# Kernel tuning notes

Measured on AMD Instinct MI355X. Metric: run time of the kernel, lower is better.

## Reference

```python
import jax, jax.numpy as jnp
import numpy as np

B, LAT, H, K = 8, 128, 1024, 294
N, E = 100000, 1600000
XSIZE = 128.0
TAU = 0.5
STEPS = 3


def setup_inputs() -> dict:
    key = jax.random.key(0)
    ks = jax.random.split(key, 20)
    s_in = 1.0 / np.sqrt(LAT)
    s_h = 1.0 / np.sqrt(H)
    inp = {
        "latent": jax.random.normal(ks[0], (B, LAT), jnp.float32),
        "W0": jax.random.normal(ks[1], (LAT, H), jnp.float32) * s_in,
        "b0": jnp.zeros((H,), jnp.float32),
        "W1": jax.random.normal(ks[2], (H, H), jnp.float32) * s_h,
        "b1": jnp.zeros((H,), jnp.float32),
        "W2": jax.random.normal(ks[3], (H, H), jnp.float32) * s_h,
        "b2": jnp.zeros((H,), jnp.float32),
        "W3": jax.random.normal(ks[4], (H, H), jnp.float32) * s_h,
        "b3": jnp.zeros((H,), jnp.float32),
        # coefficient heads use normal(1e-4) init in the source
        "Wx": jax.random.normal(ks[5], (H, K), jnp.float32) * 1e-4,
        "bx": jnp.zeros((K,), jnp.float32),
        "Wy": jax.random.normal(ks[6], (H, K), jnp.float32) * 1e-4,
        "by": jnp.zeros((K,), jnp.float32),
        "Wz": jax.random.normal(ks[7], (H, K), jnp.float32) * 1e-4,
        "bz": jnp.zeros((K,), jnp.float32),
        # precomputed Zernike/spherical basis evaluated at the N coords: [K, N]
        "Z": jax.random.normal(ks[8], (K, N), jnp.float32),
        "edge_weights": jax.random.uniform(ks[9], (E,), jnp.float32),
        "edge_index": jax.random.randint(ks[10], (2, E), 0, N, jnp.int64),
    }
    return inp


def _decode_coefficients(latent, W0, b0, W1, b1, W2, b2, W3, b3,
                         Wx, bx, Wy, by, Wz, bz):
    h = jax.nn.relu(latent @ W0 + b0)
    for W, b in ((W1, b1), (W2, b2), (W3, b3)):
        h = jax.nn.relu(h + h @ W + b)  # residual MLP block
    return h @ Wx + bx, h @ Wy + by, h @ Wz + bz  # [B, K] each


def _diffuse(flow, edge_index, edge_weights):
    """Graph diffusion smoothing of per-node vectors. flow: [B, N, 3]."""
    src, dst = edge_index[0], edge_index[1]
    deg = jax.ops.segment_sum(edge_weights, dst, num_segments=N)
    deg = jnp.maximum(deg, 1e-6)[:, None, None]  # [N,1,1]
    f = jnp.transpose(flow, (1, 0, 2))  # [N, B, 3]
    w = edge_weights[:, None, None]
    for _ in range(STEPS):
        msg = f[src] * w                                        # gather  [E,B,3]
        agg = jax.ops.segment_sum(msg, dst, num_segments=N)     # scatter [N,B,3]
        f = (1.0 - TAU) * f + TAU * agg / deg
    return jnp.transpose(f, (1, 0, 2))  # [B, N, 3]


def reference(latent, W0, b0, W1, b1, W2, b2, W3, b3,
              Wx, bx, Wy, by, Wz, bz, Z, edge_weights, edge_index):
    cx, cy, cz = _decode_coefficients(latent, W0, b0, W1, b1, W2, b2, W3, b3,
                                      Wx, bx, Wy, by, Wz, bz)
    # basis evaluation: per-axis coefficients contracted with Zernike basis
    dx = jnp.einsum("bk,kn->bn", cx, Z)
    dy = jnp.einsum("bk,kn->bn", cy, Z)
    dz = jnp.einsum("bk,kn->bn", cz, Z)
    flow = (0.5 * XSIZE) * jnp.stack([dx, dy, dz], axis=-1)  # [B, N, 3]
    flow = _diffuse(flow, edge_index, edge_weights)
    reg = 1e-4 * jnp.sqrt(jnp.sum(cx ** 2 + cy ** 2 + cz ** 2))
    return flow, reg
```

## Files before the change

### kernel.cpp

```cpp
#include <hip/hip_runtime.h>
#include <math.h>

#define BB 8
#define LAT 128
#define HH 1024
#define KK 294
#define NN 100000
#define EE 1600000
#define NSTEPS 3
#define XS_HALF 64.0f

#define NB 391
#define CS 8
#define COB 28
#define COB2 30
#define EPT 8
#define EST 200000
#define EBLK 782
#define GON 40

#define F3NB 391
#define KPAD 320

__constant__ float ccoefT[KPAD * 24];


__device__ __forceinline__ void mlp_part_body(int bid, const float* __restrict__ hin,
                                              const float* __restrict__ W,
                                              float* __restrict__ part, int jdim) {
    int it = bid & 15;
    int bs = bid >> 4;
    int tx = threadIdx.x;
    int il = tx & 63;
    int jg = tx >> 6;
    int i = it * 64 + il;
    int j0 = bs * 64;

    __shared__ float hs[8 * 64];
    for (int u = tx; u < 512; u += 256) {
        int b = u >> 6, lj = u & 63;
        hs[u] = hin[b * jdim + j0 + lj];
    }
    __syncthreads();

    float acc[8];
#pragma unroll
    for (int b = 0; b < 8; ++b) acc[b] = 0.0f;
#pragma unroll
    for (int jj = 0; jj < 16; ++jj) {
        int lj = jg * 16 + jj;
        float w = W[(size_t)(j0 + lj) * HH + i];
#pragma unroll
        for (int b = 0; b < 8; ++b) acc[b] += hs[b * 64 + lj] * w;
    }

    __shared__ float red[4][8][64];
#pragma unroll
    for (int b = 0; b < 8; ++b) red[jg][b][il] = acc[b];
    __syncthreads();
    for (int u = tx; u < 512; u += 256) {
        int b = u >> 6, ii = u & 63;
        float s = red[0][b][ii] + red[1][b][ii] + red[2][b][ii] + red[3][b][ii];
        part[(size_t)bs * 8192 + b * HH + it * 64 + ii] = s;
    }
}

__device__ __forceinline__ void mlp_comb_body(int bid, const float* __restrict__ part,
                                              int nsplit, const float* __restrict__ resid,
                                              const float* __restrict__ bias,
                                              float* __restrict__ hout) {
    int idx = bid * 256 + threadIdx.x;
    if (idx >= BB * HH) return;
    int i = idx & (HH - 1);
    float s = bias[i];
    if (resid) s += resid[idx];
    for (int bs = 0; bs < nsplit; ++bs) s += part[(size_t)bs * 8192 + idx];
    hout[idx] = fmaxf(s, 0.0f);
}

__device__ __forceinline__ void count_body(int bid, const int* __restrict__ ei,
                                           int* __restrict__ cnt, int* __restrict__ rank) {
    int gid = bid * 256 + threadIdx.x;
    if (gid >= EST) return;
    int d[EPT];
#pragma unroll
    for (int j = 0; j < EPT; ++j) d[j] = ei[EE + gid + j * EST];
#pragma unroll
    for (int j = 0; j < EPT; ++j) {
        int p = atomicAdd(&cnt[d[j]], 1);
        rank[gid + j * EST] = p;
    }
}

__device__ __forceinline__ void bsum_body(int bid, const int* __restrict__ cnt,
                                          int* __restrict__ bsum) {
    __shared__ int red[256];
    int i = bid * 256 + threadIdx.x;
    red[threadIdx.x] = (i < NN) ? cnt[i] : 0;
    __syncthreads();
    for (int off = 128; off > 0; off >>= 1) {
        if ((int)threadIdx.x < off) red[threadIdx.x] += red[threadIdx.x + off];
        __syncthreads();
    }
    if (threadIdx.x == 0) bsum[bid] = red[0];
}

__device__ __forceinline__ void bscan_body(const int* __restrict__ bsum,
                                           int* __restrict__ bpre,
                                           int* __restrict__ offs) {
    __shared__ int A[512], Bf[512];
    int t = threadIdx.x;
    A[t] = (t < NB) ? bsum[t] : 0;
    A[t + 256] = (t + 256 < NB) ? bsum[t + 256] : 0;
    __syncthreads();
    int* s = A;
    int* d = Bf;
    for (int off = 1; off < 512; off <<= 1) {
        d[t] = s[t] + ((t >= off) ? s[t - off] : 0);
        int u = t + 256;
        d[u] = s[u] + ((u >= off) ? s[u - off] : 0);
        __syncthreads();
        int* tmp = s; s = d; d = tmp;
    }
    if (t < NB) bpre[t] = (t == 0) ? 0 : s[t - 1];
    int u = t + 256;
    if (u < NB) bpre[u] = s[u - 1];
    if (t == 0) offs[NN] = s[NB - 1];
}

__device__ __forceinline__ void offs_body(int bid, const int* __restrict__ cnt,
                                          const int* __restrict__ bpre,
                                          int* __restrict__ offs) {
    __shared__ int part[256];
    int t = threadIdx.x;
    int i = bid * 256 + t;
    int v = (i < NN) ? cnt[i] : 0;
    part[t] = v;
    __syncthreads();
    for (int off = 1; off < 256; off <<= 1) {
        int u = (t >= off) ? part[t - off] : 0;
        __syncthreads();
        part[t] += u;
        __syncthreads();
    }
    if (i < NN) offs[i] = bpre[bid] + part[t] - v;
}

__device__ __forceinline__ void fill_body(int bid, const int* __restrict__ ei,
                                          const float* __restrict__ ew,
                                          const int* __restrict__ offs,
                                          const int* __restrict__ rank,
                                          int2* __restrict__ csr) {
    int gid = bid * 256 + threadIdx.x;
    if (gid >= EST) return;
    int s[EPT], d[EPT], r[EPT];
    float w[EPT];
#pragma unroll
    for (int j = 0; j < EPT; ++j) {
        int e = gid + j * EST;
        s[j] = ei[e];
        d[j] = ei[EE + e];
        w[j] = ew[e];
        r[j] = rank[e];
    }
#pragma unroll
    for (int j = 0; j < EPT; ++j) {
        int p = offs[d[j]] + r[j];
        int2 v;
        v.x = s[j];
        v.y = __float_as_int(w[j]);
        csr[p] = v;
    }
}

__device__ __forceinline__ void flow3_body(int bid, const float* __restrict__ Z,
                                           float* __restrict__ fout) {
    __shared__ float zl[4][4][8][64];

    int t = threadIdx.x;
    int lane = t & 63;
    int wu = __builtin_amdgcn_readfirstlane(t >> 6);

    int n = bid * 256 + (wu << 6) + lane;
    int nn = (n < NN) ? n : (NN - 1);
    const float* zn = Z + nn;

    float acc[24];
#pragma unroll
    for (int j = 0; j < 24; ++j) acc[j] = 0.0f;

    auto issue = [&](int cp) {
        int b = cp & 3;
#pragma unroll
        for (int d = 0; d < 8; ++d) {
            int r = cp * 8 + d;
            int rz = (r < KK) ? r : (KK - 1);
            __builtin_amdgcn_global_load_lds(
                (__attribute__((address_space(1))) unsigned int*)(zn + (size_t)rz * NN),
                (__attribute__((address_space(3))) unsigned int*)(&zl[wu][b][d][0]),
                4, 0, 0);
        }
    };

    issue(0); issue(1); issue(2);

#pragma unroll 1
    for (int c = 0; c < 37; ++c) {
        issue(c + 3);
        asm volatile("s_waitcnt vmcnt(24)" ::: "memory");
        __builtin_amdgcn_sched_barrier(0);
        int b = c & 3;
#pragma unroll
        for (int d = 0; d < 8; ++d) {
            float z = zl[wu][b][d][lane];
            const float* cf = &ccoefT[(c * 8 + d) * 24];
#pragma unroll
            for (int j = 0; j < 24; ++j) acc[j] = fmaf(cf[j], z, acc[j]);
        }
    }

    if (n < NN) {
        float buf4[24];
#pragma unroll
        for (int j = 0; j < 24; ++j) buf4[j] = XS_HALF * acc[j];
        float4* fr = (float4*)(fout + (size_t)n * 24);
#pragma unroll
        for (int q = 0; q < 6; ++q) fr[q] = ((const float4*)buf4)[q];
    }
}

__device__ __forceinline__ void reg_body(const float* __restrict__ coef,
                                         float* __restrict__ out_reg) {
    __shared__ float red[256];
    float s = 0.0f;
    for (int i = threadIdx.x; i < 3 * BB * KK; i += 256) {
        float v = coef[i];
        s += v * v;
    }
    red[threadIdx.x] = s;
    __syncthreads();
    for (int off = 128; off > 0; off >>= 1) {
        if ((int)threadIdx.x < off) red[threadIdx.x] += red[threadIdx.x + off];
        __syncthreads();
    }
    if (threadIdx.x == 0) out_reg[0] = 1e-4f * sqrtf(red[0]);
}


__global__ void K1_mlp0_count(const float* __restrict__ latent, const float* __restrict__ W0,
                              float* __restrict__ part, const int* __restrict__ ei,
                              int* __restrict__ cnt, int* __restrict__ rank) {
    if (blockIdx.x < 32) mlp_part_body(blockIdx.x, latent, W0, part, LAT);
    else count_body(blockIdx.x - 32, ei, cnt, rank);
}

__global__ void K2_comb0_bsum(const float* __restrict__ part, const float* __restrict__ b0,
                              float* __restrict__ hout, const int* __restrict__ cnt,
                              int* __restrict__ bsum) {
    if (blockIdx.x < 32) mlp_comb_body(blockIdx.x, part, 2, nullptr, b0, hout);
    else bsum_body(blockIdx.x - 32, cnt, bsum);
}

__global__ void K3_bscan_mlp1(const int* __restrict__ bsum, int* __restrict__ bpre,
                              int* __restrict__ offs, const float* __restrict__ hin,
                              const float* __restrict__ W1, float* __restrict__ part) {
    if (blockIdx.x == 0) bscan_body(bsum, bpre, offs);
    else mlp_part_body(blockIdx.x - 1, hin, W1, part, HH);
}

__global__ void K4_comb1_offs(const float* __restrict__ part, const float* __restrict__ resid,
                              const float* __restrict__ b1, float* __restrict__ hout,
                              const int* __restrict__ cnt, const int* __restrict__ bpre,
                              int* __restrict__ offs) {
    if (blockIdx.x < 32) mlp_comb_body(blockIdx.x, part, 16, resid, b1, hout);
    else offs_body(blockIdx.x - 32, cnt, bpre, offs);
}

__global__ void K5_mlp2_fill(const float* __restrict__ hin, const float* __restrict__ W2,
                             float* __restrict__ part, const int* __restrict__ ei,
                             const float* __restrict__ ew, const int* __restrict__ offs,
                             const int* __restrict__ rank, int2* __restrict__ csr) {
    if (blockIdx.x < 256) mlp_part_body(blockIdx.x, hin, W2, part, HH);
    else fill_body(blockIdx.x - 256, ei, ew, offs, rank, csr);
}

__global__ void K6_comb2(const float* __restrict__ part, const float* __restrict__ resid,
                         const float* __restrict__ bias, float* __restrict__ hout) {
    mlp_comb_body(blockIdx.x, part, 16, resid, bias, hout);
}

__global__ void K_mlp_part3(const float* __restrict__ hin, const float* __restrict__ W,
                            float* __restrict__ part) {
    mlp_part_body(blockIdx.x, hin, W, part, HH);
}

__global__ void K_mlp_comb(const float* __restrict__ part, const float* __restrict__ resid,
                           const float* __restrict__ bias, float* __restrict__ hout) {
    mlp_comb_body(blockIdx.x, part, 16, resid, bias, hout);
}

__global__ void k_coef_part(const float* __restrict__ h,
                            const float* __restrict__ Wx,
                            const float* __restrict__ Wy,
                            const float* __restrict__ Wz,
                            float* __restrict__ cpart) {
    int s = blockIdx.x / COB;
    int blk = blockIdx.x % COB;
    int o = blk * 256 + threadIdx.x;
    if (o >= 3 * BB * KK) return;
    int t = o / (BB * KK);
    int r = o % (BB * KK);
    int b = r / KK, k = r % KK;
    const float* W = (t == 0) ? Wx : ((t == 1) ? Wy : Wz);
    const float* hr = h + b * HH;
    int j0 = s * 128;
    float acc = 0.0f;
#pragma unroll 8
    for (int j = 0; j < 128; ++j) acc += hr[j0 + j] * W[(size_t)(j0 + j) * KK + k];
    cpart[(size_t)s * 7056 + o] = acc;
}

__global__ void k_coef_comb(const float* __restrict__ cpart,
                            const float* __restrict__ bx,
                            const float* __restrict__ by,
                            const float* __restrict__ bz,
                            float* __restrict__ coefT) {
    int o = blockIdx.x * 256 + threadIdx.x;
    if (o >= KPAD * 24) return;
    if (o >= 3 * BB * KK) {
        coefT[o] = 0.0f;
        return;
    }
    int t = o / (BB * KK);
    int r = o % (BB * KK);
    int b = r / KK;
    int k = r % KK;
    float s = ((t == 0) ? bx : ((t == 1) ? by : bz))[k];
#pragma unroll
    for (int i = 0; i < CS; ++i) s += cpart[(size_t)i * 7056 + o];
    coefT[k * 24 + b * 3 + t] = s;
}

__global__ void K11_flow_reg(const float* __restrict__ coefT, const float* __restrict__ Z,
                             float* __restrict__ fout, float* __restrict__ out_reg) {
    if (blockIdx.x < F3NB) flow3_body(blockIdx.x, Z, fout);
    else reg_body(coefT, out_reg);
}

__global__ void k_gather(const int* __restrict__ offs, const int2* __restrict__ csr,
                         const float* __restrict__ fin, float* __restrict__ fout) {
    int idx = blockIdx.x * 256 + threadIdx.x;
    if (idx >= NN * 6) return;
    int n = idx / 6;
    int q = idx - n * 6;
    int beg = offs[n], end = offs[n + 1];
    const float4* f4 = (const float4*)fin;
    float4 acc = make_float4(0.f, 0.f, 0.f, 0.f);
    float wsum = 0.0f;
    int i = beg;
    for (; i + 4 <= end; i += 4) {
        int2 e[4];
#pragma unroll
        for (int u = 0; u < 4; ++u) e[u] = csr[i + u];
        float4 v[4];
#pragma unroll
        for (int u = 0; u < 4; ++u) v[u] = f4[(size_t)e[u].x * 6 + q];
#pragma unroll
        for (int u = 0; u < 4; ++u) {
            float w = __int_as_float(e[u].y);
            wsum += w;
            acc.x += w * v[u].x;
            acc.y += w * v[u].y;
            acc.z += w * v[u].z;
            acc.w += w * v[u].w;
        }
    }
    for (; i < end; ++i) {
        int2 e = csr[i];
        float w = __int_as_float(e.y);
        float4 fv = f4[(size_t)e.x * 6 + q];
        wsum += w;
        acc.x += w * fv.x;
        acc.y += w * fv.y;
        acc.z += w * fv.z;
        acc.w += w * fv.w;
    }
    float inv = 0.5f / fmaxf(wsum, 1e-6f);
    float4 fo = f4[(size_t)n * 6 + q];
    float4 r;
    r.x = 0.5f * fo.x + inv * acc.x;
    r.y = 0.5f * fo.y + inv * acc.y;
    r.z = 0.5f * fo.z + inv * acc.z;
    r.w = 0.5f * fo.w + inv * acc.w;
    ((float4*)fout)[(size_t)n * 6 + q] = r;
}

__global__ void k_gather_out(const int* __restrict__ offs, const int2* __restrict__ csr,
                             const float* __restrict__ fin, float* __restrict__ out) {
    __shared__ float ls[GON * 24];
    int t = threadIdx.x;
    int n0 = blockIdx.x * GON;
    if (t < GON * 6) {
        int ln = t / 6, q = t - 6 * ln;
        int n = n0 + ln;
        if (n < NN) {
            int beg = offs[n], end = offs[n + 1];
            const float4* f4 = (const float4*)fin;
            float4 acc = make_float4(0.f, 0.f, 0.f, 0.f);
            float wsum = 0.0f;
            int i = beg;
            for (; i + 4 <= end; i += 4) {
                int2 e[4];
#pragma unroll
                for (int u = 0; u < 4; ++u) e[u] = csr[i + u];
                float4 v[4];
#pragma unroll
                for (int u = 0; u < 4; ++u) v[u] = f4[(size_t)e[u].x * 6 + q];
#pragma unroll
                for (int u = 0; u < 4; ++u) {
                    float w = __int_as_float(e[u].y);
                    wsum += w;
                    acc.x += w * v[u].x;
                    acc.y += w * v[u].y;
                    acc.z += w * v[u].z;
                    acc.w += w * v[u].w;
                }
            }
            for (; i < end; ++i) {
                int2 e = csr[i];
                float w = __int_as_float(e.y);
                float4 fv = f4[(size_t)e.x * 6 + q];
                wsum += w;
                acc.x += w * fv.x;
                acc.y += w * fv.y;
                acc.z += w * fv.z;
                acc.w += w * fv.w;
            }
            float inv = 0.5f / fmaxf(wsum, 1e-6f);
            float4 fo = f4[(size_t)n * 6 + q];
            float* d = &ls[ln * 24 + q * 4];
            d[0] = 0.5f * fo.x + inv * acc.x;
            d[1] = 0.5f * fo.y + inv * acc.y;
            d[2] = 0.5f * fo.z + inv * acc.z;
            d[3] = 0.5f * fo.w + inv * acc.w;
        }
    }
    __syncthreads();
    int cnt = NN - n0; if (cnt > GON) cnt = GON;
    int per_b = cnt * 3;
    for (int b = 0; b < BB; ++b) {
        for (int u = t; u < per_b; u += 256) {
            int n = u / 3;
            int c = u - 3 * n;
            out[(size_t)b * (NN * 3) + (size_t)n0 * 3 + u] = ls[n * 24 + b * 3 + c];
        }
    }
}

extern "C" void kernel_launch(void* const* d_in, const int* in_sizes, int n_in,
                              void* d_out, int out_size, void* d_ws, size_t ws_size,
                              hipStream_t stream) {
    const float* latent = (const float*)d_in[0];
    const float* W0 = (const float*)d_in[1];
    const float* b0 = (const float*)d_in[2];
    const float* W1 = (const float*)d_in[3];
    const float* b1 = (const float*)d_in[4];
    const float* W2 = (const float*)d_in[5];
    const float* b2 = (const float*)d_in[6];
    const float* W3 = (const float*)d_in[7];
    const float* b3 = (const float*)d_in[8];
    const float* Wx = (const float*)d_in[9];
    const float* bx = (const float*)d_in[10];
    const float* Wy = (const float*)d_in[11];
    const float* by = (const float*)d_in[12];
    const float* Wz = (const float*)d_in[13];
    const float* bz = (const float*)d_in[14];
    const float* Z  = (const float*)d_in[15];
    const float* ew = (const float*)d_in[16];
    const int*   ei = (const int*)d_in[17];
    float* out = (float*)d_out;

    float* p = (float*)d_ws;
    float* h_a     = p; p += 8192;
    float* h_b     = p; p += 8192;
    float* hp      = p; p += 16 * 8192;
    float* coef    = p; p += KPAD * 24;
    float* cpart   = p; p += CS * 7056;
    int*   cnt     = (int*)p; p += 100000;
    int*   offs    = (int*)p; p += 100016;
    int*   bsum    = (int*)p; p += 512;
    int*   bpre    = (int*)p; p += 512;
    int*   rank    = (int*)p; p += 1600000;
    int2*  csr     = (int2*)p; p += 2 * 1600000;
    float* fpart   = p; p += (size_t)2 * NN * 24;

    hipMemsetAsync(cnt, 0, NN * sizeof(int), stream);

    K1_mlp0_count<<<32 + EBLK, 256, 0, stream>>>(latent, W0, hp, ei, cnt, rank);
    K2_comb0_bsum<<<32 + NB, 256, 0, stream>>>(hp, b0, h_a, cnt, bsum);
    K3_bscan_mlp1<<<1 + 256, 256, 0, stream>>>(bsum, bpre, offs, h_a, W1, hp);
    K4_comb1_offs<<<32 + NB, 256, 0, stream>>>(hp, h_a, b1, h_b, cnt, bpre, offs);
    K5_mlp2_fill<<<256 + EBLK, 256, 0, stream>>>(h_b, W2, hp, ei, ew, offs, rank, csr);
    K6_comb2<<<32, 256, 0, stream>>>(hp, h_b, b2, h_a);
    K_mlp_part3<<<256, 256, 0, stream>>>(h_a, W3, hp);
    K_mlp_comb<<<32, 256, 0, stream>>>(hp, h_a, b3, h_b);
    k_coef_part<<<COB * CS, 256, 0, stream>>>(h_b, Wx, Wy, Wz, cpart);
    k_coef_comb<<<COB2, 256, 0, stream>>>(cpart, bx, by, bz, coef);
    hipMemcpyToSymbolAsync(HIP_SYMBOL(ccoefT), coef, KPAD * 24 * sizeof(float), 0,
                           hipMemcpyDeviceToDevice, stream);
    K11_flow_reg<<<F3NB + 1, 256, 0, stream>>>(coef, Z, fpart, out + (size_t)BB * NN * 3);

    float* f0 = fpart;
    float* f1 = fpart + (size_t)NN * 24;
    k_gather<<<(NN * 6 + 255) / 256, 256, 0, stream>>>(offs, csr, f0, f1);
    k_gather<<<(NN * 6 + 255) / 256, 256, 0, stream>>>(offs, csr, f1, f0);
    k_gather_out<<<(NN + GON - 1) / GON, 256, 0, stream>>>(offs, csr, f0, out);
}
```

Baseline: 502.4 us.

## Move CSR build from MLP kernels into flow kernel and separate launches

Takes the CSR construction stages (count, block-sum, scan, offsets, fill) out of the MLP-chain kernels. The count stage now shares a launch with the flow basis evaluation and the reg reduction. The other stages run as their own launches after it. The MLP layers become generic part/comb kernels launched with small grids. This changes which work overlaps: the CSR build now overlaps the memory-heavy Z contraction rather than the latency-bound MLP, and it adds four extra launches on the critical path.

```diff
diff --git a/kernel.cpp b/kernel.cpp
--- a/kernel.cpp
+++ b/kernel.cpp
@@ -247,56 +247,15 @@
 }
 
 
-__global__ void K1_mlp0_count(const float* __restrict__ latent, const float* __restrict__ W0,
-                              float* __restrict__ part, const int* __restrict__ ei,
-                              int* __restrict__ cnt, int* __restrict__ rank) {
-    if (blockIdx.x < 32) mlp_part_body(blockIdx.x, latent, W0, part, LAT);
-    else count_body(blockIdx.x - 32, ei, cnt, rank);
-}
-
-__global__ void K2_comb0_bsum(const float* __restrict__ part, const float* __restrict__ b0,
-                              float* __restrict__ hout, const int* __restrict__ cnt,
-                              int* __restrict__ bsum) {
-    if (blockIdx.x < 32) mlp_comb_body(blockIdx.x, part, 2, nullptr, b0, hout);
-    else bsum_body(blockIdx.x - 32, cnt, bsum);
-}
-
-__global__ void K3_bscan_mlp1(const int* __restrict__ bsum, int* __restrict__ bpre,
-                              int* __restrict__ offs, const float* __restrict__ hin,
-                              const float* __restrict__ W1, float* __restrict__ part) {
-    if (blockIdx.x == 0) bscan_body(bsum, bpre, offs);
-    else mlp_part_body(blockIdx.x - 1, hin, W1, part, HH);
-}
-
-__global__ void K4_comb1_offs(const float* __restrict__ part, const float* __restrict__ resid,
-                              const float* __restrict__ b1, float* __restrict__ hout,
-                              const int* __restrict__ cnt, const int* __restrict__ bpre,
-                              int* __restrict__ offs) {
-    if (blockIdx.x < 32) mlp_comb_body(blockIdx.x, part, 16, resid, b1, hout);
-    else offs_body(blockIdx.x - 32, cnt, bpre, offs);
-}
-
-__global__ void K5_mlp2_fill(const float* __restrict__ hin, const float* __restrict__ W2,
-                             float* __restrict__ part, const int* __restrict__ ei,
-                             const float* __restrict__ ew, const int* __restrict__ offs,
-                             const int* __restrict__ rank, int2* __restrict__ csr) {
-    if (blockIdx.x < 256) mlp_part_body(blockIdx.x, hin, W2, part, HH);
-    else fill_body(blockIdx.x - 256, ei, ew, offs, rank, csr);
-}
-
-__global__ void K6_comb2(const float* __restrict__ part, const float* __restrict__ resid,
-                         const float* __restrict__ bias, float* __restrict__ hout) {
-    mlp_comb_body(blockIdx.x, part, 16, resid, bias, hout);
-}
-
-__global__ void K_mlp_part3(const float* __restrict__ hin, const float* __restrict__ W,
-                            float* __restrict__ part) {
-    mlp_part_body(blockIdx.x, hin, W, part, HH);
-}
-
-__global__ void K_mlp_comb(const float* __restrict__ part, const float* __restrict__ resid,
-                           const float* __restrict__ bias, float* __restrict__ hout) {
-    mlp_comb_body(blockIdx.x, part, 16, resid, bias, hout);
+__global__ void K_part(const float* __restrict__ hin, const float* __restrict__ W,
+                       float* __restrict__ part, int jdim) {
+    mlp_part_body(blockIdx.x, hin, W, part, jdim);
+}
+
+__global__ void K_comb(const float* __restrict__ part, int nsplit,
+                       const float* __restrict__ resid, const float* __restrict__ bias,
+                       float* __restrict__ hout) {
+    mlp_comb_body(blockIdx.x, part, nsplit, resid, bias, hout);
 }
 
 __global__ void k_coef_part(const float* __restrict__ h,
@@ -341,10 +300,33 @@
     coefT[k * 24 + b * 3 + t] = s;
 }
 
-__global__ void K11_flow_reg(const float* __restrict__ coefT, const float* __restrict__ Z,
-                             float* __restrict__ fout, float* __restrict__ out_reg) {
+__global__ void K_flow_count_reg(const float* __restrict__ Z, float* __restrict__ fout,
+                                 const int* __restrict__ ei, int* __restrict__ cnt,
+                                 int* __restrict__ rank, const float* __restrict__ coefT,
+                                 float* __restrict__ out_reg) {
     if (blockIdx.x < F3NB) flow3_body(blockIdx.x, Z, fout);
+    else if (blockIdx.x < F3NB + EBLK) count_body(blockIdx.x - F3NB, ei, cnt, rank);
     else reg_body(coefT, out_reg);
+}
+
+__global__ void K_bsum(const int* __restrict__ cnt, int* __restrict__ bsum) {
+    bsum_body(blockIdx.x, cnt, bsum);
+}
+
+__global__ void K_bscan(const int* __restrict__ bsum, int* __restrict__ bpre,
+                        int* __restrict__ offs) {
+    bscan_body(bsum, bpre, offs);
+}
+
+__global__ void K_offs(const int* __restrict__ cnt, const int* __restrict__ bpre,
+                       int* __restrict__ offs) {
+    offs_body(blockIdx.x, cnt, bpre, offs);
+}
+
+__global__ void K_fill(const int* __restrict__ ei, const float* __restrict__ ew,
+                       const int* __restrict__ offs, const int* __restrict__ rank,
+                       int2* __restrict__ csr) {
+    fill_body(blockIdx.x, ei, ew, offs, rank, csr);
 }
 
 __global__ void k_gather(const int* __restrict__ offs, const int2* __restrict__ csr,
@@ -496,22 +478,29 @@
 
     hipMemsetAsync(cnt, 0, NN * sizeof(int), stream);
 
-    K1_mlp0_count<<<32 + EBLK, 256, 0, stream>>>(latent, W0, hp, ei, cnt, rank);
-    K2_comb0_bsum<<<32 + NB, 256, 0, stream>>>(hp, b0, h_a, cnt, bsum);
-    K3_bscan_mlp1<<<1 + 256, 256, 0, stream>>>(bsum, bpre, offs, h_a, W1, hp);
-    K4_comb1_offs<<<32 + NB, 256, 0, stream>>>(hp, h_a, b1, h_b, cnt, bpre, offs);
-    K5_mlp2_fill<<<256 + EBLK, 256, 0, stream>>>(h_b, W2, hp, ei, ew, offs, rank, csr);
-    K6_comb2<<<32, 256, 0, stream>>>(hp, h_b, b2, h_a);
-    K_mlp_part3<<<256, 256, 0, stream>>>(h_a, W3, hp);
-    K_mlp_comb<<<32, 256, 0, stream>>>(hp, h_a, b3, h_b);
+    K_part<<<32, 256, 0, stream>>>(latent, W0, hp, LAT);
+    K_comb<<<32, 256, 0, stream>>>(hp, 2, nullptr, b0, h_a);
+    K_part<<<256, 256, 0, stream>>>(h_a, W1, hp, HH);
+    K_comb<<<32, 256, 0, stream>>>(hp, 16, h_a, b1, h_b);
+    K_part<<<256, 256, 0, stream>>>(h_b, W2, hp, HH);
+    K_comb<<<32, 256, 0, stream>>>(hp, 16, h_b, b2, h_a);
+    K_part<<<256, 256, 0, stream>>>(h_a, W3, hp, HH);
+    K_comb<<<32, 256, 0, stream>>>(hp, 16, h_a, b3, h_b);
     k_coef_part<<<COB * CS, 256, 0, stream>>>(h_b, Wx, Wy, Wz, cpart);
     k_coef_comb<<<COB2, 256, 0, stream>>>(cpart, bx, by, bz, coef);
     hipMemcpyToSymbolAsync(HIP_SYMBOL(ccoefT), coef, KPAD * 24 * sizeof(float), 0,
                            hipMemcpyDeviceToDevice, stream);
-    K11_flow_reg<<<F3NB + 1, 256, 0, stream>>>(coef, Z, fpart, out + (size_t)BB * NN * 3);
 
     float* f0 = fpart;
     float* f1 = fpart + (size_t)NN * 24;
+    K_flow_count_reg<<<F3NB + EBLK + 1, 256, 0, stream>>>(Z, f0, ei, cnt, rank, coef,
+                                                          out + (size_t)BB * NN * 3);
+
+    K_bsum<<<NB, 256, 0, stream>>>(cnt, bsum);
+    K_bscan<<<1, 256, 0, stream>>>(bsum, bpre, offs);
+    K_offs<<<NB, 256, 0, stream>>>(cnt, bpre, offs);
+    K_fill<<<EBLK, 256, 0, stream>>>(ei, ew, offs, rank, csr);
+
     k_gather<<<(NN * 6 + 255) / 256, 256, 0, stream>>>(offs, csr, f0, f1);
     k_gather<<<(NN * 6 + 255) / 256, 256, 0, stream>>>(offs, csr, f1, f0);
     k_gather_out<<<(NN + GON - 1) / GON, 256, 0, stream>>>(offs, csr, f0, out);
```

Result: no change. 509.3 us (+1.4%).

## Spread CSR construction across all MLP kernels to overlap with the decoder

Applied to the files above, without the earlier changes.

The edge-count atomics are split into four chunks of blocks and co-launched with the first four MLP kernels. The block-sum, scan and offset stages now ride along with the later MLP layers, and the CSR fill is merged into the flow-evaluation kernel. The aim is to hide the graph-preprocessing latency behind the small, under-occupied MLP launches and balance work per launch. In exchange, the fill now shares a launch with the memory-heavy Z contraction, which could add contention there.

```diff
diff --git a/kernel.cpp b/kernel.cpp
--- a/kernel.cpp
+++ b/kernel.cpp
@@ -17,6 +17,7 @@
 #define EPT 8
 #define EST 200000
 #define EBLK 782
+#define QA 196
 #define GON 40
 
 #define F3NB 391
@@ -78,9 +79,9 @@
     hout[idx] = fmaxf(s, 0.0f);
 }
 
-__device__ __forceinline__ void count_body(int bid, const int* __restrict__ ei,
+__device__ __forceinline__ void count_body(int gbid, const int* __restrict__ ei,
                                            int* __restrict__ cnt, int* __restrict__ rank) {
-    int gid = bid * 256 + threadIdx.x;
+    int gid = gbid * 256 + threadIdx.x;
     if (gid >= EST) return;
     int d[EPT];
 #pragma unroll
@@ -247,56 +248,60 @@
 }
 
 
-__global__ void K1_mlp0_count(const float* __restrict__ latent, const float* __restrict__ W0,
-                              float* __restrict__ part, const int* __restrict__ ei,
-                              int* __restrict__ cnt, int* __restrict__ rank) {
+__global__ void K1_mlp0_cnt(const float* __restrict__ latent, const float* __restrict__ W0,
+                            float* __restrict__ part, const int* __restrict__ ei,
+                            int* __restrict__ cnt, int* __restrict__ rank) {
     if (blockIdx.x < 32) mlp_part_body(blockIdx.x, latent, W0, part, LAT);
     else count_body(blockIdx.x - 32, ei, cnt, rank);
 }
 
-__global__ void K2_comb0_bsum(const float* __restrict__ part, const float* __restrict__ b0,
-                              float* __restrict__ hout, const int* __restrict__ cnt,
-                              int* __restrict__ bsum) {
+__global__ void K2_comb0_cnt(const float* __restrict__ part, const float* __restrict__ b0,
+                             float* __restrict__ hout, const int* __restrict__ ei,
+                             int* __restrict__ cnt, int* __restrict__ rank) {
     if (blockIdx.x < 32) mlp_comb_body(blockIdx.x, part, 2, nullptr, b0, hout);
-    else bsum_body(blockIdx.x - 32, cnt, bsum);
-}
-
-__global__ void K3_bscan_mlp1(const int* __restrict__ bsum, int* __restrict__ bpre,
-                              int* __restrict__ offs, const float* __restrict__ hin,
-                              const float* __restrict__ W1, float* __restrict__ part) {
-    if (blockIdx.x == 0) bscan_body(bsum, bpre, offs);
-    else mlp_part_body(blockIdx.x - 1, hin, W1, part, HH);
-}
-
-__global__ void K4_comb1_offs(const float* __restrict__ part, const float* __restrict__ resid,
-                              const float* __restrict__ b1, float* __restrict__ hout,
-                              const int* __restrict__ cnt, const int* __restrict__ bpre,
-                              int* __restrict__ offs) {
+    else count_body(blockIdx.x - 32 + QA, ei, cnt, rank);
+}
+
+__global__ void K3_mlp1_cnt(const float* __restrict__ hin, const float* __restrict__ W1,
+                            float* __restrict__ part, const int* __restrict__ ei,
+                            int* __restrict__ cnt, int* __restrict__ rank) {
+    if (blockIdx.x < 256) mlp_part_body(blockIdx.x, hin, W1, part, HH);
+    else count_body(blockIdx.x - 256 + 2 * QA, ei, cnt, rank);
+}
+
+__global__ void K4_comb1_cnt(const float* __restrict__ part, const float* __restrict__ resid,
+                             const float* __restrict__ b1, float* __restrict__ hout,
+                             const int* __restrict__ ei, int* __restrict__ cnt,
+                             int* __restrict__ rank) {
     if (blockIdx.x < 32) mlp_comb_body(blockIdx.x, part, 16, resid, b1, hout);
-    else offs_body(blockIdx.x - 32, cnt, bpre, offs);
-}
-
-__global__ void K5_mlp2_fill(const float* __restrict__ hin, const float* __restrict__ W2,
-                             float* __restrict__ part, const int* __restrict__ ei,
-                             const float* __restrict__ ew, const int* __restrict__ offs,
-                             const int* __restrict__ rank, int2* __restrict__ csr) {
+    else count_body(blockIdx.x - 32 + 3 * QA, ei, cnt, rank);
+}
+
+__global__ void K5_mlp2_bsum(const float* __restrict__ hin, const float* __restrict__ W2,
+                             float* __restrict__ part, const int* __restrict__ cnt,
+                             int* __restrict__ bsum) {
     if (blockIdx.x < 256) mlp_part_body(blockIdx.x, hin, W2, part, HH);
-    else fill_body(blockIdx.x - 256, ei, ew, offs, rank, csr);
-}
-
-__global__ void K6_comb2(const float* __restrict__ part, const float* __restrict__ resid,
-                         const float* __restrict__ bias, float* __restrict__ hout) {
-    mlp_comb_body(blockIdx.x, part, 16, resid, bias, hout);
-}
-
-__global__ void K_mlp_part3(const float* __restrict__ hin, const float* __restrict__ W,
-                            float* __restrict__ part) {
-    mlp_part_body(blockIdx.x, hin, W, part, HH);
-}
-
-__global__ void K_mlp_comb(const float* __restrict__ part, const float* __restrict__ resid,
-                           const float* __restrict__ bias, float* __restrict__ hout) {
-    mlp_comb_body(blockIdx.x, part, 16, resid, bias, hout);
+    else bsum_body(blockIdx.x - 256, cnt, bsum);
+}
+
+__global__ void K6_comb2_bscan(const float* __restrict__ part, const float* __restrict__ resid,
+                               const float* __restrict__ b2, float* __restrict__ hout,
+                               const int* __restrict__ bsum, int* __restrict__ bpre,
+                               int* __restrict__ offs) {
+    if (blockIdx.x < 32) mlp_comb_body(blockIdx.x, part, 16, resid, b2, hout);
+    else bscan_body(bsum, bpre, offs);
+}
+
+__global__ void K7_mlp3_offs(const float* __restrict__ hin, const float* __restrict__ W3,
+                             float* __restrict__ part, const int* __restrict__ cnt,
+                             const int* __restrict__ bpre, int* __restrict__ offs) {
+    if (blockIdx.x < 256) mlp_part_body(blockIdx.x, hin, W3, part, HH);
+    else offs_body(blockIdx.x - 256, cnt, bpre, offs);
+}
+
+__global__ void K8_comb3(const float* __restrict__ part, const float* __restrict__ resid,
+                         const float* __restrict__ b3, float* __restrict__ hout) {
+    mlp_comb_body(blockIdx.x, part, 16, resid, b3, hout);
 }
 
 __global__ void k_coef_part(const float* __restrict__ h,
@@ -341,9 +346,13 @@
     coefT[k * 24 + b * 3 + t] = s;
 }
 
-__global__ void K11_flow_reg(const float* __restrict__ coefT, const float* __restrict__ Z,
-                             float* __restrict__ fout, float* __restrict__ out_reg) {
+__global__ void K_flow_fill_reg(const float* __restrict__ Z, float* __restrict__ fout,
+                                const int* __restrict__ ei, const float* __restrict__ ew,
+                                const int* __restrict__ offs, const int* __restrict__ rank,
+                                int2* __restrict__ csr, const float* __restrict__ coefT,
+                                float* __restrict__ out_reg) {
     if (blockIdx.x < F3NB) flow3_body(blockIdx.x, Z, fout);
+    else if (blockIdx.x < F3NB + EBLK) fill_body(blockIdx.x - F3NB, ei, ew, offs, rank, csr);
     else reg_body(coefT, out_reg);
 }
 
@@ -496,22 +505,24 @@
 
     hipMemsetAsync(cnt, 0, NN * sizeof(int), stream);
 
-    K1_mlp0_count<<<32 + EBLK, 256, 0, stream>>>(latent, W0, hp, ei, cnt, rank);
-    K2_comb0_bsum<<<32 + NB, 256, 0, stream>>>(hp, b0, h_a, cnt, bsum);
-    K3_bscan_mlp1<<<1 + 256, 256, 0, stream>>>(bsum, bpre, offs, h_a, W1, hp);
-    K4_comb1_offs<<<32 + NB, 256, 0, stream>>>(hp, h_a, b1, h_b, cnt, bpre, offs);
-    K5_mlp2_fill<<<256 + EBLK, 256, 0, stream>>>(h_b, W2, hp, ei, ew, offs, rank, csr);
-    K6_comb2<<<32, 256, 0, stream>>>(hp, h_b, b2, h_a);
-    K_mlp_part3<<<256, 256, 0, stream>>>(h_a, W3, hp);
-    K_mlp_comb<<<32, 256, 0, stream>>>(hp, h_a, b3, h_b);
+    K1_mlp0_cnt<<<32 + QA, 256, 0, stream>>>(latent, W0, hp, ei, cnt, rank);
+    K2_comb0_cnt<<<32 + QA, 256, 0, stream>>>(hp, b0, h_a, ei, cnt, rank);
+    K3_mlp1_cnt<<<256 + QA, 256, 0, stream>>>(h_a, W1, hp, ei, cnt, rank);
+    K4_comb1_cnt<<<32 + (EBLK - 3 * QA), 256, 0, stream>>>(hp, h_a, b1, h_b, ei, cnt, rank);
+    K5_mlp2_bsum<<<256 + NB, 256, 0, stream>>>(h_b, W2, hp, cnt, bsum);
+    K6_comb2_bscan<<<32 + 1, 256, 0, stream>>>(hp, h_b, b2, h_a, bsum, bpre, offs);
+    K7_mlp3_offs<<<256 + NB, 256, 0, stream>>>(h_a, W3, hp, cnt, bpre, offs);
+    K8_comb3<<<32, 256, 0, stream>>>(hp, h_a, b3, h_b);
     k_coef_part<<<COB * CS, 256, 0, stream>>>(h_b, Wx, Wy, Wz, cpart);
     k_coef_comb<<<COB2, 256, 0, stream>>>(cpart, bx, by, bz, coef);
     hipMemcpyToSymbolAsync(HIP_SYMBOL(ccoefT), coef, KPAD * 24 * sizeof(float), 0,
                            hipMemcpyDeviceToDevice, stream);
-    K11_flow_reg<<<F3NB + 1, 256, 0, stream>>>(coef, Z, fpart, out + (size_t)BB * NN * 3);
 
     float* f0 = fpart;
     float* f1 = fpart + (size_t)NN * 24;
+    K_flow_fill_reg<<<F3NB + EBLK + 1, 256, 0, stream>>>(Z, f0, ei, ew, offs, rank, csr,
+                                                         coef, out + (size_t)BB * NN * 3);
+
     k_gather<<<(NN * 6 + 255) / 256, 256, 0, stream>>>(offs, csr, f0, f1);
     k_gather<<<(NN * 6 + 255) / 256, 256, 0, stream>>>(offs, csr, f1, f0);
     k_gather_out<<<(NN + GON - 1) / GON, 256, 0, stream>>>(offs, csr, f0, out);
```

Result: faster. 486.8 us (-3.1%).
